# Kernel tuning notes

Measured on AMD Instinct MI355X. Metric: run time of the kernel, lower is better.

## Reference

```python
import jax, jax.numpy as jnp
import numpy as np

B, N, F, E = 256, 784, 1, 6272   # batch, nodes, in-features, edges
C = 32                            # GraphConv channels
H = 512                           # fc1 hidden units
N_OUT = 10


def setup_inputs() -> dict:
    key = jax.random.key(0)
    ks = jax.random.split(key, 12)
    x = jax.random.normal(ks[0], (B, N, F), dtype=jnp.float32)
    edge_row = jax.random.randint(ks[1], (E,), 0, N, dtype=jnp.int32)
    edge_col = jax.random.randint(ks[2], (E,), 0, N, dtype=jnp.int32)
    edge_val = jax.random.uniform(ks[3], (E,), dtype=jnp.float32)
    # GraphConv weights (Glorot-ish scale)
    W1 = jax.random.normal(ks[4], (F, C), dtype=jnp.float32) * 0.5
    b1 = jnp.zeros((C,), dtype=jnp.float32)
    W2 = jax.random.normal(ks[5], (C, C), dtype=jnp.float32) * 0.18
    b2 = jnp.zeros((C,), dtype=jnp.float32)
    # MLP head
    Wf1 = jax.random.normal(ks[6], (N * C, H), dtype=jnp.float32) * 0.01
    bf1 = jnp.zeros((H,), dtype=jnp.float32)
    Wf2 = jax.random.normal(ks[7], (H, N_OUT), dtype=jnp.float32) * 0.04
    bf2 = jnp.zeros((N_OUT,), dtype=jnp.float32)
    return {"x": x, "edge_row": edge_row, "edge_col": edge_col, "edge_val": edge_val,
            "W1": W1, "b1": b1, "W2": W2, "b2": b2,
            "Wf1": Wf1, "bf1": bf1, "Wf2": Wf2, "bf2": bf2}


def _spmm(h, row, col, val):
    # h: [B, N, C]; sparse fltr (COO) @ h per batch element
    msg = jnp.swapaxes(h[:, col, :], 0, 1) * val[:, None, None]      # [E, B, C]
    agg = jax.ops.segment_sum(msg, row, num_segments=N)              # [N, B, C]
    return jnp.swapaxes(agg, 0, 1)                                   # [B, N, C]


def reference(x, edge_row, edge_col, edge_val, W1, b1, W2, b2, Wf1, bf1, Wf2, bf2):
    # GraphConv 1: elu(fltr @ x @ W1 + b1)
    h = jax.nn.elu(_spmm(x, edge_row, edge_col, edge_val) @ W1 + b1)
    # GraphConv 2
    h = jax.nn.elu(_spmm(h, edge_row, edge_col, edge_val) @ W2 + b2)
    # Flatten -> Dense(512, relu) -> Dense(10, softmax)
    flat = h.reshape(B, N * C)
    z = jax.nn.relu(flat @ Wf1 + bf1)
    return jax.nn.softmax(z @ Wf2 + bf2, axis=-1)
```

## Files before the change

kernel.cpp:

```cpp
#include <hip/hip_runtime.h>
#include <hip/hip_bf16.h>

#define B_ 256
#define N_ 784
#define E_ 6272
#define C_ 32
#define H_ 512
#define NK 25088
#define BC 8192
#define S_SPLIT 28
#define KCHUNK 896
#define KSTEPS 28

typedef __attribute__((ext_vector_type(8))) short short8;
typedef __attribute__((ext_vector_type(4))) float f32x4;

__device__ __forceinline__ float elu1(float v) {
  return v > 0.f ? v : (__expf(v) - 1.f);
}

__device__ __forceinline__ unsigned short bf16b(float v) {
  __hip_bfloat16 h = __float2bfloat16(v);
  return *reinterpret_cast<unsigned short*>(&h);
}

__device__ __forceinline__ unsigned int pk2(float lo, float hi) {
  return (unsigned int)bf16b(lo) | ((unsigned int)bf16b(hi) << 16);
}

__device__ __forceinline__ void acc2(unsigned u, float val, float& a0, float& a1) {
  float lo = __uint_as_float(u << 16);
  float hi = __uint_as_float(u & 0xffff0000u);
  a0 = fmaf(val, lo, a0);
  a1 = fmaf(val, hi, a1);
}

__global__ __launch_bounds__(1024) void k_build_csr(
    const int* __restrict__ erow, const int* __restrict__ ecol,
    const float* __restrict__ eval,
    int* __restrict__ row_ptr, int* __restrict__ col_s, float* __restrict__ val_s) {
  __shared__ int cnt[N_];
  __shared__ int off[N_];
  __shared__ int bufA[1024];
  __shared__ int bufB[1024];
  const int t = threadIdx.x;
  if (t < N_) cnt[t] = 0;
  __syncthreads();
  for (int e = t; e < E_; e += 1024) atomicAdd(&cnt[erow[e]], 1);
  __syncthreads();
  bufA[t] = (t < N_) ? cnt[t] : 0;
  __syncthreads();
  int* src = bufA; int* dst = bufB;
  for (int d = 1; d < 1024; d <<= 1) {
    int v = src[t];
    if (t >= d) v += src[t - d];
    dst[t] = v;
    __syncthreads();
    int* tmp = src; src = dst; dst = tmp;
  }
  if (t < N_) {
    int ex = src[t] - cnt[t];
    off[t] = ex;
    row_ptr[t] = ex;
  }
  if (t == 0) row_ptr[N_] = E_;
  __syncthreads();
  for (int e = t; e < E_; e += 1024) {
    int r = erow[e];
    int p = atomicAdd(&off[r], 1);
    col_s[p] = ecol[e];
    val_s[p] = eval[e];
  }
}

__global__ __launch_bounds__(256) void k_xt(
    const float* __restrict__ x, float* __restrict__ xT) {
  __shared__ float tile[32][33];
  int n0 = blockIdx.x * 32, b0 = blockIdx.y * 32;
  int t = threadIdx.x;
  int ni = t & 31, bi = t >> 5;
#pragma unroll
  for (int it = 0; it < 4; ++it) {
    int n = n0 + ni;
    if (n < N_) tile[ni][bi + it * 8] = x[(b0 + bi + it * 8) * N_ + n];
  }
  __syncthreads();
  int bj = t & 31, nj = t >> 5;
#pragma unroll
  for (int it = 0; it < 4; ++it) {
    int n = n0 + nj + it * 8;
    if (n < N_) xT[n * B_ + b0 + bj] = tile[nj + it * 8][bj];
  }
}

__global__ __launch_bounds__(256) void k_gc1(
    const float* __restrict__ xT, const int* __restrict__ row_ptr,
    const int* __restrict__ col_s, const float* __restrict__ val_s,
    const float* __restrict__ W1, const float* __restrict__ b1,
    __hip_bfloat16* __restrict__ h1) {
  __shared__ int lc[64];
  __shared__ float lv[64];
  int n = blockIdx.x, t = threadIdx.x;
  int e0 = row_ptr[n], deg = row_ptr[n + 1] - e0;
  float agg = 0.f;
  for (int base = 0; base < deg; base += 64) {
    int m = min(64, deg - base);
    __syncthreads();
    if (t < m) { lc[t] = col_s[e0 + base + t]; lv[t] = val_s[e0 + base + t]; }
    __syncthreads();
    for (int e = 0; e < m; ++e)
      agg = fmaf(lv[e], xT[lc[e] * B_ + t], agg);
  }
  union { unsigned int u[16]; uint4 v[4]; } ob;
#pragma unroll
  for (int c = 0; c < C_; c += 2) {
    float o0 = elu1(fmaf(agg, W1[c], b1[c]));
    float o1 = elu1(fmaf(agg, W1[c + 1], b1[c + 1]));
    ob.u[c >> 1] = pk2(o0, o1);
  }
  uint4* dst = reinterpret_cast<uint4*>(h1 + (size_t)n * BC + t * C_);
#pragma unroll
  for (int j = 0; j < 4; ++j) dst[j] = ob.v[j];
}

__global__ __launch_bounds__(256) void k_gc2(
    const __hip_bfloat16* __restrict__ h1, const int* __restrict__ row_ptr,
    const int* __restrict__ col_s, const float* __restrict__ val_s,
    const float* __restrict__ W2, const float* __restrict__ b2,
    __hip_bfloat16* __restrict__ flat) {
  __shared__ int lc[64];
  __shared__ float lv[64];
  int n = blockIdx.x, t = threadIdx.x;
  int e0 = row_ptr[n], deg = row_ptr[n + 1] - e0;
  float acc[C_];
#pragma unroll
  for (int c = 0; c < C_; ++c) acc[c] = 0.f;
  for (int base = 0; base < deg; base += 64) {
    int m = min(64, deg - base);
    __syncthreads();
    if (t < m) { lc[t] = col_s[e0 + base + t]; lv[t] = val_s[e0 + base + t]; }
    __syncthreads();
    for (int e = 0; e < m; ++e) {
      float val = lv[e];
      const uint4* hp = reinterpret_cast<const uint4*>(
          h1 + (size_t)lc[e] * BC + t * C_);
#pragma unroll
      for (int j = 0; j < 4; ++j) {
        uint4 v = hp[j];
        acc2(v.x, val, acc[j * 8 + 0], acc[j * 8 + 1]);
        acc2(v.y, val, acc[j * 8 + 2], acc[j * 8 + 3]);
        acc2(v.z, val, acc[j * 8 + 4], acc[j * 8 + 5]);
        acc2(v.w, val, acc[j * 8 + 6], acc[j * 8 + 7]);
      }
    }
  }
  union { unsigned int u[16]; uint4 v[4]; } ob;
#pragma unroll
  for (int c2 = 0; c2 < C_; c2 += 2) {
    float o0 = b2[c2], o1 = b2[c2 + 1];
#pragma unroll
    for (int c = 0; c < C_; ++c) {
      o0 = fmaf(acc[c], W2[c * C_ + c2], o0);
      o1 = fmaf(acc[c], W2[c * C_ + c2 + 1], o1);
    }
    ob.u[c2 >> 1] = pk2(elu1(o0), elu1(o1));
  }
  uint4* dst = reinterpret_cast<uint4*>(flat + (size_t)t * NK + n * C_);
#pragma unroll
  for (int j = 0; j < 4; ++j) dst[j] = ob.v[j];
}

__global__ __launch_bounds__(512) void k_fc1(
    const __hip_bfloat16* __restrict__ flat, const float* __restrict__ Wf1,
    float* __restrict__ partial) {
  __shared__ unsigned short Alds[2][256][40];
  __shared__ unsigned short Blds[2][64][40];
  int s = blockIdx.x >> 3, nt = blockIdx.x & 7;
  int n0 = nt * 64;
  int k0 = s * KCHUNK;
  int tid = threadIdx.x;
  int w = tid >> 6, l = tid & 63;
  int r = l & 15, g = l >> 4;
  int wm = (w & 3) * 64;
  int wn = (w >> 2) * 32;
  int am = tid >> 1, ah = (tid & 1) * 16;
  bool doB = tid < 256;
  int bkp = (tid >> 4) & 15, bn4 = (tid & 15) * 4;

  f32x4 acc[4][2];
#pragma unroll
  for (int i = 0; i < 4; ++i)
#pragma unroll
    for (int j = 0; j < 2; ++j) acc[i][j] = (f32x4){0.f, 0.f, 0.f, 0.f};

  int4 aX0, aX1, aY0, aY1;
  float4 bX0, bX1, bY0, bY1;

#define GLOAD_A(step, v0, v1) do {                                            \
    const int4* _p = reinterpret_cast<const int4*>(                           \
        flat + (size_t)am * NK + k0 + (step) * 32 + ah);                      \
    v0 = _p[0]; v1 = _p[1];                                                   \
  } while (0)
#define GLOAD_B(step, r0, r1) do {                                            \
    if (doB) {                                                                \
      const float* _b = Wf1 + (size_t)(k0 + (step) * 32 + 2 * bkp) * H_       \
                        + n0 + bn4;                                           \
      r0 = *reinterpret_cast<const float4*>(_b);                              \
      r1 = *reinterpret_cast<const float4*>(_b + H_);                         \
    }                                                                         \
  } while (0)
#define WRITE_LDS(buf, v0, v1, r0, r1) do {                                   \
    int4* _ad = reinterpret_cast<int4*>(&Alds[buf][am][ah]);                  \
    _ad[0] = v0; _ad[1] = v1;                                                 \
    if (doB) {                                                                \
      *reinterpret_cast<unsigned int*>(&Blds[buf][bn4 + 0][2 * bkp]) = pk2(r0.x, r1.x); \
      *reinterpret_cast<unsigned int*>(&Blds[buf][bn4 + 1][2 * bkp]) = pk2(r0.y, r1.y); \
      *reinterpret_cast<unsigned int*>(&Blds[buf][bn4 + 2][2 * bkp]) = pk2(r0.z, r1.z); \
      *reinterpret_cast<unsigned int*>(&Blds[buf][bn4 + 3][2 * bkp]) = pk2(r0.w, r1.w); \
    }                                                                         \
  } while (0)
#define MFMA_STEP(buf) do {                                                   \
    short8 _a[4];                                                             \
    _Pragma("unroll")                                                         \
    for (int fm = 0; fm < 4; ++fm)                                            \
      _a[fm] = *reinterpret_cast<const short8*>(&Alds[buf][wm + fm * 16 + r][g * 8]); \
    _Pragma("unroll")                                                         \
    for (int fn = 0; fn < 2; ++fn) {                                          \
      short8 _bb = *reinterpret_cast<const short8*>(&Blds[buf][wn + fn * 16 + r][g * 8]); \
      _Pragma("unroll")                                                       \
      for (int fm = 0; fm < 4; ++fm)                                          \
        acc[fm][fn] = __builtin_amdgcn_mfma_f32_16x16x32_bf16(_a[fm], _bb, acc[fm][fn], 0, 0, 0); \
    }                                                                         \
  } while (0)

  GLOAD_A(0, aX0, aX1); GLOAD_B(0, bX0, bX1);
  GLOAD_A(1, aY0, aY1); GLOAD_B(1, bY0, bY1);
  WRITE_LDS(0, aX0, aX1, bX0, bX1);
  __syncthreads();

  for (int s2 = 0; s2 < KSTEPS; s2 += 2) {
    WRITE_LDS(1, aY0, aY1, bY0, bY1);
    if (s2 + 2 < KSTEPS) { GLOAD_A(s2 + 2, aX0, aX1); GLOAD_B(s2 + 2, bX0, bX1); }
    MFMA_STEP(0);
    __syncthreads();
    if (s2 + 2 < KSTEPS) WRITE_LDS(0, aX0, aX1, bX0, bX1);
    if (s2 + 3 < KSTEPS) { GLOAD_A(s2 + 3, aY0, aY1); GLOAD_B(s2 + 3, bY0, bY1); }
    MFMA_STEP(1);
    __syncthreads();
  }

#undef GLOAD_A
#undef GLOAD_B
#undef WRITE_LDS
#undef MFMA_STEP

  float* p = partial + (size_t)s * (256 * 512);
#pragma unroll
  for (int fm = 0; fm < 4; ++fm)
#pragma unroll
    for (int fn = 0; fn < 2; ++fn)
#pragma unroll
      for (int q = 0; q < 4; ++q) {
        int m = wm + fm * 16 + g * 4 + q;
        int n = n0 + wn + fn * 16 + r;
        p[m * 512 + n] = acc[fm][fn][q];
      }
}

__global__ __launch_bounds__(512) void k_head(
    const float* __restrict__ partial, const float* __restrict__ bf1,
    const float* __restrict__ Wf2, const float* __restrict__ bf2,
    float* __restrict__ out) {
  __shared__ float red[8][12];
  int b = blockIdx.x;
  int t = threadIdx.x;
  float v = bf1[t];
#pragma unroll
  for (int s = 0; s < S_SPLIT; ++s)
    v += partial[(size_t)s * (256 * 512) + b * 512 + t];
  v = fmaxf(v, 0.f);
  float pacc[10];
#pragma unroll
  for (int j = 0; j < 10; ++j) pacc[j] = v * Wf2[t * 10 + j];
#pragma unroll
  for (int j = 0; j < 10; ++j)
#pragma unroll
    for (int d = 32; d > 0; d >>= 1)
      pacc[j] += __shfl_down(pacc[j], d);
  int wv = t >> 6, ln = t & 63;
  if (ln == 0) {
#pragma unroll
    for (int j = 0; j < 10; ++j) red[wv][j] = pacc[j];
  }
  __syncthreads();
  if (t == 0) {
    float lg[10];
    float m = -1e30f;
#pragma unroll
    for (int j = 0; j < 10; ++j) {
      float z = bf2[j];
#pragma unroll
      for (int wq = 0; wq < 8; ++wq) z += red[wq][j];
      lg[j] = z;
      m = fmaxf(m, z);
    }
    float sum = 0.f;
#pragma unroll
    for (int j = 0; j < 10; ++j) { lg[j] = __expf(lg[j] - m); sum += lg[j]; }
    float inv = 1.f / sum;
#pragma unroll
    for (int j = 0; j < 10; ++j) out[b * 10 + j] = lg[j] * inv;
  }
}

extern "C" void kernel_launch(void* const* d_in, const int* in_sizes, int n_in,
                              void* d_out, int out_size, void* d_ws, size_t ws_size,
                              hipStream_t stream) {
  const float* x    = (const float*)d_in[0];
  const int*   erow = (const int*)d_in[1];
  const int*   ecol = (const int*)d_in[2];
  const float* ev   = (const float*)d_in[3];
  const float* W1   = (const float*)d_in[4];
  const float* b1   = (const float*)d_in[5];
  const float* W2   = (const float*)d_in[6];
  const float* b2   = (const float*)d_in[7];
  const float* Wf1  = (const float*)d_in[8];
  const float* bf1  = (const float*)d_in[9];
  const float* Wf2  = (const float*)d_in[10];
  const float* bf2  = (const float*)d_in[11];
  float* out = (float*)d_out;

  char* ws = (char*)d_ws;
  const size_t partial_bytes = (size_t)S_SPLIT * 256 * 512 * 4;
  const size_t flat_bytes    = (size_t)B_ * NK * 2;
  float* partial = (float*)ws;
  float* xT = (float*)ws;
  __hip_bfloat16* h1 = (__hip_bfloat16*)(ws + 802816);
  __hip_bfloat16* flat = (__hip_bfloat16*)(ws + partial_bytes);
  char* tail = ws + partial_bytes + flat_bytes;
  int*   row_ptr = (int*)tail;
  int*   col_s   = (int*)(tail + 3152);
  float* val_s   = (float*)(tail + 3152 + E_ * 4);

  hipLaunchKernelGGL(k_build_csr, dim3(1), dim3(1024), 0, stream,
                     erow, ecol, ev, row_ptr, col_s, val_s);
  hipLaunchKernelGGL(k_xt, dim3(25, 8), dim3(256), 0, stream, x, xT);
  hipLaunchKernelGGL(k_gc1, dim3(N_), dim3(256), 0, stream,
                     xT, row_ptr, col_s, val_s, W1, b1, h1);
  hipLaunchKernelGGL(k_gc2, dim3(N_), dim3(256), 0, stream,
                     h1, row_ptr, col_s, val_s, W2, b2, flat);
  hipLaunchKernelGGL(k_fc1, dim3(S_SPLIT * 8), dim3(512), 0, stream,
                     flat, Wf1, partial);
  hipLaunchKernelGGL(k_head, dim3(B_), dim3(512), 0, stream,
                     partial, bf1, Wf2, bf2, out);
}
```

Baseline: 94.17 us.

## Fuse CSR build with transpose and retile fc1 split-K for more blocks

Merges the CSR construction and the x transpose into one launch, with block 0 building the CSR and the remaining 1024-thread blocks each transposing a 32x32 tile. The fc1 GEMM is retiled from 256x64 tiles with 512 threads to 128x64 tiles with 256 threads, and the split-K factor rises to 56 when the workspace is large enough, so the grid grows from 224 to as many as 896 blocks. The B-tile load now reads eight scalar rows per thread and writes one 16-byte LDS store. This trades more partial-sum traffic and a longer reduction in the head kernel for better CU occupancy and one fewer launch.

```diff
diff --git a/kernel.cpp b/kernel.cpp
--- a/kernel.cpp
+++ b/kernel.cpp
@@ -8,9 +8,6 @@
 #define H_ 512
 #define NK 25088
 #define BC 8192
-#define S_SPLIT 28
-#define KCHUNK 896
-#define KSTEPS 28
 
 typedef __attribute__((ext_vector_type(8))) short short8;
 typedef __attribute__((ext_vector_type(4))) float f32x4;
@@ -35,61 +32,55 @@
   a1 = fmaf(val, hi, a1);
 }
 
-__global__ __launch_bounds__(1024) void k_build_csr(
+__global__ __launch_bounds__(1024) void k_prep(
     const int* __restrict__ erow, const int* __restrict__ ecol,
-    const float* __restrict__ eval,
-    int* __restrict__ row_ptr, int* __restrict__ col_s, float* __restrict__ val_s) {
-  __shared__ int cnt[N_];
-  __shared__ int off[N_];
-  __shared__ int bufA[1024];
-  __shared__ int bufB[1024];
+    const float* __restrict__ eval, const float* __restrict__ x,
+    int* __restrict__ row_ptr, int* __restrict__ col_s, float* __restrict__ val_s,
+    float* __restrict__ xT) {
   const int t = threadIdx.x;
-  if (t < N_) cnt[t] = 0;
-  __syncthreads();
-  for (int e = t; e < E_; e += 1024) atomicAdd(&cnt[erow[e]], 1);
-  __syncthreads();
-  bufA[t] = (t < N_) ? cnt[t] : 0;
-  __syncthreads();
-  int* src = bufA; int* dst = bufB;
-  for (int d = 1; d < 1024; d <<= 1) {
-    int v = src[t];
-    if (t >= d) v += src[t - d];
-    dst[t] = v;
-    __syncthreads();
-    int* tmp = src; src = dst; dst = tmp;
-  }
-  if (t < N_) {
-    int ex = src[t] - cnt[t];
-    off[t] = ex;
-    row_ptr[t] = ex;
-  }
-  if (t == 0) row_ptr[N_] = E_;
-  __syncthreads();
-  for (int e = t; e < E_; e += 1024) {
-    int r = erow[e];
-    int p = atomicAdd(&off[r], 1);
-    col_s[p] = ecol[e];
-    val_s[p] = eval[e];
-  }
-}
-
-__global__ __launch_bounds__(256) void k_xt(
-    const float* __restrict__ x, float* __restrict__ xT) {
-  __shared__ float tile[32][33];
-  int n0 = blockIdx.x * 32, b0 = blockIdx.y * 32;
-  int t = threadIdx.x;
-  int ni = t & 31, bi = t >> 5;
-#pragma unroll
-  for (int it = 0; it < 4; ++it) {
+  if (blockIdx.x == 0) {
+    __shared__ int cnt[N_];
+    __shared__ int off[N_];
+    __shared__ int bufA[1024];
+    __shared__ int bufB[1024];
+    if (t < N_) cnt[t] = 0;
+    __syncthreads();
+    for (int e = t; e < E_; e += 1024) atomicAdd(&cnt[erow[e]], 1);
+    __syncthreads();
+    bufA[t] = (t < N_) ? cnt[t] : 0;
+    __syncthreads();
+    int* src = bufA; int* dst = bufB;
+    for (int d = 1; d < 1024; d <<= 1) {
+      int v = src[t];
+      if (t >= d) v += src[t - d];
+      dst[t] = v;
+      __syncthreads();
+      int* tmp = src; src = dst; dst = tmp;
+    }
+    if (t < N_) {
+      int ex = src[t] - cnt[t];
+      off[t] = ex;
+      row_ptr[t] = ex;
+    }
+    if (t == 0) row_ptr[N_] = E_;
+    __syncthreads();
+    for (int e = t; e < E_; e += 1024) {
+      int r = erow[e];
+      int p = atomicAdd(&off[r], 1);
+      col_s[p] = ecol[e];
+      val_s[p] = eval[e];
+    }
+  } else {
+    __shared__ float tile[32][33];
+    int bid = blockIdx.x - 1;
+    int n0 = (bid % 25) * 32, b0 = (bid / 25) * 32;
+    int ni = t & 31, bi = t >> 5;
     int n = n0 + ni;
-    if (n < N_) tile[ni][bi + it * 8] = x[(b0 + bi + it * 8) * N_ + n];
-  }
-  __syncthreads();
-  int bj = t & 31, nj = t >> 5;
-#pragma unroll
-  for (int it = 0; it < 4; ++it) {
-    int n = n0 + nj + it * 8;
-    if (n < N_) xT[n * B_ + b0 + bj] = tile[nj + it * 8][bj];
+    if (n < N_) tile[ni][bi] = x[(b0 + bi) * N_ + n];
+    __syncthreads();
+    int nj = t >> 5, bj = t & 31;
+    int nw = n0 + nj;
+    if (nw < N_) xT[nw * B_ + b0 + bj] = tile[nj][bj];
   }
 }
 
@@ -170,22 +161,23 @@
   for (int j = 0; j < 4; ++j) dst[j] = ob.v[j];
 }
 
-__global__ __launch_bounds__(512) void k_fc1(
+__global__ __launch_bounds__(256) void k_fc1(
     const __hip_bfloat16* __restrict__ flat, const float* __restrict__ Wf1,
-    float* __restrict__ partial) {
-  __shared__ unsigned short Alds[2][256][40];
+    float* __restrict__ partial, int ksteps) {
+  __shared__ unsigned short Alds[2][128][40];
   __shared__ unsigned short Blds[2][64][40];
-  int s = blockIdx.x >> 3, nt = blockIdx.x & 7;
-  int n0 = nt * 64;
-  int k0 = s * KCHUNK;
+  int bid = blockIdx.x;
+  int s = bid >> 4, r16 = bid & 15;
+  int m0 = (r16 & 1) * 128;
+  int n0 = (r16 >> 1) * 64;
+  int k0 = s * ksteps * 32;
   int tid = threadIdx.x;
   int w = tid >> 6, l = tid & 63;
   int r = l & 15, g = l >> 4;
-  int wm = (w & 3) * 64;
-  int wn = (w >> 2) * 32;
+  int wm = (w & 1) * 64;
+  int wn = (w >> 1) * 32;
   int am = tid >> 1, ah = (tid & 1) * 16;
-  bool doB = tid < 256;
-  int bkp = (tid >> 4) & 15, bn4 = (tid & 15) * 4;
+  int bn = tid & 63, boct = tid >> 6;
 
   f32x4 acc[4][2];
 #pragma unroll
@@ -194,30 +186,26 @@
     for (int j = 0; j < 2; ++j) acc[i][j] = (f32x4){0.f, 0.f, 0.f, 0.f};
 
   int4 aX0, aX1, aY0, aY1;
-  float4 bX0, bX1, bY0, bY1;
+  float fX[8], fY[8];
 
 #define GLOAD_A(step, v0, v1) do {                                            \
     const int4* _p = reinterpret_cast<const int4*>(                           \
-        flat + (size_t)am * NK + k0 + (step) * 32 + ah);                      \
+        flat + (size_t)(m0 + am) * NK + k0 + (step) * 32 + ah);               \
     v0 = _p[0]; v1 = _p[1];                                                   \
   } while (0)
-#define GLOAD_B(step, r0, r1) do {                                            \
-    if (doB) {                                                                \
-      const float* _b = Wf1 + (size_t)(k0 + (step) * 32 + 2 * bkp) * H_       \
-                        + n0 + bn4;                                           \
-      r0 = *reinterpret_cast<const float4*>(_b);                              \
-      r1 = *reinterpret_cast<const float4*>(_b + H_);                         \
-    }                                                                         \
+#define GLOAD_B(step, f) do {                                                 \
+    const float* _b = Wf1 + (size_t)(k0 + (step) * 32 + boct * 8) * H_        \
+                      + n0 + bn;                                              \
+    _Pragma("unroll")                                                         \
+    for (int i = 0; i < 8; ++i) f[i] = _b[i * H_];                            \
   } while (0)
-#define WRITE_LDS(buf, v0, v1, r0, r1) do {                                   \
+#define WRITE_LDS(buf, v0, v1, f) do {                                        \
     int4* _ad = reinterpret_cast<int4*>(&Alds[buf][am][ah]);                  \
     _ad[0] = v0; _ad[1] = v1;                                                 \
-    if (doB) {                                                                \
-      *reinterpret_cast<unsigned int*>(&Blds[buf][bn4 + 0][2 * bkp]) = pk2(r0.x, r1.x); \
-      *reinterpret_cast<unsigned int*>(&Blds[buf][bn4 + 1][2 * bkp]) = pk2(r0.y, r1.y); \
-      *reinterpret_cast<unsigned int*>(&Blds[buf][bn4 + 2][2 * bkp]) = pk2(r0.z, r1.z); \
-      *reinterpret_cast<unsigned int*>(&Blds[buf][bn4 + 3][2 * bkp]) = pk2(r0.w, r1.w); \
-    }                                                                         \
+    uint4 _bu;                                                                \
+    _bu.x = pk2(f[0], f[1]); _bu.y = pk2(f[2], f[3]);                         \
+    _bu.z = pk2(f[4], f[5]); _bu.w = pk2(f[6], f[7]);                         \
+    *reinterpret_cast<uint4*>(&Blds[buf][bn][boct * 8]) = _bu;                \
   } while (0)
 #define MFMA_STEP(buf) do {                                                   \
     short8 _a[4];                                                             \
@@ -233,18 +221,18 @@
     }                                                                         \
   } while (0)
 
-  GLOAD_A(0, aX0, aX1); GLOAD_B(0, bX0, bX1);
-  GLOAD_A(1, aY0, aY1); GLOAD_B(1, bY0, bY1);
-  WRITE_LDS(0, aX0, aX1, bX0, bX1);
+  GLOAD_A(0, aX0, aX1); GLOAD_B(0, fX);
+  GLOAD_A(1, aY0, aY1); GLOAD_B(1, fY);
+  WRITE_LDS(0, aX0, aX1, fX);
   __syncthreads();
 
-  for (int s2 = 0; s2 < KSTEPS; s2 += 2) {
-    WRITE_LDS(1, aY0, aY1, bY0, bY1);
-    if (s2 + 2 < KSTEPS) { GLOAD_A(s2 + 2, aX0, aX1); GLOAD_B(s2 + 2, bX0, bX1); }
+  for (int s2 = 0; s2 < ksteps; s2 += 2) {
+    WRITE_LDS(1, aY0, aY1, fY);
+    if (s2 + 2 < ksteps) { GLOAD_A(s2 + 2, aX0, aX1); GLOAD_B(s2 + 2, fX); }
     MFMA_STEP(0);
     __syncthreads();
-    if (s2 + 2 < KSTEPS) WRITE_LDS(0, aX0, aX1, bX0, bX1);
-    if (s2 + 3 < KSTEPS) { GLOAD_A(s2 + 3, aY0, aY1); GLOAD_B(s2 + 3, bY0, bY1); }
+    if (s2 + 2 < ksteps) WRITE_LDS(0, aX0, aX1, fX);
+    if (s2 + 3 < ksteps) { GLOAD_A(s2 + 3, aY0, aY1); GLOAD_B(s2 + 3, fY); }
     MFMA_STEP(1);
     __syncthreads();
   }
@@ -261,7 +249,7 @@
     for (int fn = 0; fn < 2; ++fn)
 #pragma unroll
       for (int q = 0; q < 4; ++q) {
-        int m = wm + fm * 16 + g * 4 + q;
+        int m = m0 + wm + fm * 16 + g * 4 + q;
         int n = n0 + wn + fn * 16 + r;
         p[m * 512 + n] = acc[fm][fn][q];
       }
@@ -270,13 +258,12 @@
 __global__ __launch_bounds__(512) void k_head(
     const float* __restrict__ partial, const float* __restrict__ bf1,
     const float* __restrict__ Wf2, const float* __restrict__ bf2,
-    float* __restrict__ out) {
+    float* __restrict__ out, int S) {
   __shared__ float red[8][12];
   int b = blockIdx.x;
   int t = threadIdx.x;
   float v = bf1[t];
-#pragma unroll
-  for (int s = 0; s < S_SPLIT; ++s)
+  for (int s = 0; s < S; ++s)
     v += partial[(size_t)s * (256 * 512) + b * 512 + t];
   v = fmaxf(v, 0.f);
   float pacc[10];
@@ -330,9 +317,13 @@
   const float* bf2  = (const float*)d_in[11];
   float* out = (float*)d_out;
 
+  const size_t flat_bytes = (size_t)B_ * NK * 2;
+  size_t need56 = (size_t)56 * 256 * 512 * 4 + flat_bytes + 65536;
+  int S = (ws_size >= need56) ? 56 : 28;
+  int ksteps = NK / (S * 32);
+  size_t partial_bytes = (size_t)S * 256 * 512 * 4;
+
   char* ws = (char*)d_ws;
-  const size_t partial_bytes = (size_t)S_SPLIT * 256 * 512 * 4;
-  const size_t flat_bytes    = (size_t)B_ * NK * 2;
   float* partial = (float*)ws;
   float* xT = (float*)ws;
   __hip_bfloat16* h1 = (__hip_bfloat16*)(ws + 802816);
@@ -342,15 +333,14 @@
   int*   col_s   = (int*)(tail + 3152);
   float* val_s   = (float*)(tail + 3152 + E_ * 4);
 
-  hipLaunchKernelGGL(k_build_csr, dim3(1), dim3(1024), 0, stream,
-                     erow, ecol, ev, row_ptr, col_s, val_s);
-  hipLaunchKernelGGL(k_xt, dim3(25, 8), dim3(256), 0, stream, x, xT);
+  hipLaunchKernelGGL(k_prep, dim3(1 + 25 * 8), dim3(1024), 0, stream,
+                     erow, ecol, ev, x, row_ptr, col_s, val_s, xT);
   hipLaunchKernelGGL(k_gc1, dim3(N_), dim3(256), 0, stream,
                      xT, row_ptr, col_s, val_s, W1, b1, h1);
   hipLaunchKernelGGL(k_gc2, dim3(N_), dim3(256), 0, stream,
                      h1, row_ptr, col_s, val_s, W2, b2, flat);
-  hipLaunchKernelGGL(k_fc1, dim3(S_SPLIT * 8), dim3(512), 0, stream,
-                     flat, Wf1, partial);
+  hipLaunchKernelGGL(k_fc1, dim3(16 * S), dim3(256), 0, stream,
+                     flat, Wf1, partial, ksteps);
   hipLaunchKernelGGL(k_head, dim3(B_), dim3(512), 0, stream,
-                     partial, bf1, Wf2, bf2, out);
-}
+                     partial, bf1, Wf2, bf2, out, S);
+}
```

After: 104.7 us. +11.2%, slower.
